# Kernel tuning notes

Measured on AMD Instinct MI355X. Metric: run time of the kernel, lower is better.

## Reference

```python
import jax, jax.numpy as jnp
import numpy as np

T_OUT = 12  # num_timesteps_output


def setup_inputs() -> dict:
    key = jax.random.key(0)
    ks = jax.random.split(key, 12)
    B, N, T, F = 32, 325, 12, 2
    C, H = 10, 64
    s = 0.08  # weight init scale (~1/sqrt(H)) to keep gates in sane range
    return {
        "A": jnp.zeros((N, N), jnp.float32),
        "X": jax.random.normal(ks[0], (B, N, T, F), jnp.float32),
        "enc_Wih": jax.random.normal(ks[1], (C, 3 * H, F), jnp.float32) * s,
        "enc_Whh": jax.random.normal(ks[2], (C, 3 * H, H), jnp.float32) * s,
        "enc_bih": jax.random.normal(ks[3], (C, 3 * H), jnp.float32) * s,
        "enc_bhh": jax.random.normal(ks[4], (C, 3 * H), jnp.float32) * s,
        "dec_Wih": jax.random.normal(ks[5], (C, 3 * H, 1), jnp.float32) * s,
        "dec_Whh": jax.random.normal(ks[6], (C, 3 * H, H), jnp.float32) * s,
        "dec_bih": jax.random.normal(ks[7], (C, 3 * H), jnp.float32) * s,
        "dec_bhh": jax.random.normal(ks[8], (C, 3 * H), jnp.float32) * s,
        "lin_W": jax.random.normal(ks[9], (C, 1, H), jnp.float32) * s,
        "lin_b": jax.random.normal(ks[10], (C, 1), jnp.float32) * s,
        "embed": jax.random.normal(ks[11], (N, C), jnp.float32),
    }


def _gru_update(gi, gh, h, H):
    # PyTorch GRU gate order: r, z, n
    r = jax.nn.sigmoid(gi[..., :H] + gh[..., :H])
    z = jax.nn.sigmoid(gi[..., H:2 * H] + gh[..., H:2 * H])
    n = jnp.tanh(gi[..., 2 * H:] + r * gh[..., 2 * H:])
    return (1.0 - z) * n + z * h


def reference(A, X, enc_Wih, enc_Whh, enc_bih, enc_bhh,
              dec_Wih, dec_Whh, dec_bih, dec_bhh, lin_W, lin_b, embed):
    B, N, T, F = X.shape
    C = enc_Wih.shape[0]
    H = enc_Whh.shape[-1]
    BN = B * N

    # (T, BN, F): time-major, batch*nodes flattened (matches X.view(-1,T,F).permute(1,0,2))
    Xs = jnp.transpose(X.reshape(BN, T, F), (1, 0, 2))

    def enc_step(h, x_t):  # h: (C, BN, H), x_t: (BN, F)
        gi = jnp.einsum('bf,cgf->cbg', x_t, enc_Wih) + enc_bih[:, None, :]
        gh = jnp.einsum('cbh,cgh->cbg', h, enc_Whh) + enc_bhh[:, None, :]
        return _gru_update(gi, gh, h, H), None

    h0 = jnp.zeros((C, BN, H), X.dtype)
    h_enc, _ = jax.lax.scan(enc_step, h0, Xs)  # (C, BN, H)

    # initial decoder input: last observed value of feature 0
    lv0 = jnp.broadcast_to(Xs[-1, :, 0][None, :, None], (C, BN, 1))

    def dec_step(carry, _):
        h, lv = carry
        gi = jnp.einsum('cbf,cgf->cbg', lv, dec_Wih) + dec_bih[:, None, :]
        gh = jnp.einsum('cbh,cgh->cbg', h, dec_Whh) + dec_bhh[:, None, :]
        h = _gru_update(gi, gh, h, H)
        value = jnp.einsum('cbh,coh->cbo', h, lin_W) + lin_b[:, None, :]  # (C, BN, 1)
        # original does last_value = value.detach()
        return (h, jax.lax.stop_gradient(value)), value

    (_, _), vals = jax.lax.scan(dec_step, (h_enc, lv0), None, length=T_OUT)
    # vals: (T_out, C, BN, 1) -> (B, N, T_out, C)
    out = jnp.transpose(vals[..., 0], (2, 0, 1)).reshape(B, N, T_OUT, C)

    weight = jax.nn.softmax(embed, axis=-1)  # (N, C)
    return jnp.einsum('bntc,nc->bnt', out, weight)
```

## Files before the change

kernel.cpp:

```cpp
#include <hip/hip_runtime.h>
#include <math.h>

#define N_     325
#define BN_    10400
#define OUTSZ_ (BN_*12)


typedef _Float16 h8v  __attribute__((ext_vector_type(8)));
typedef float    f4v  __attribute__((ext_vector_type(4)));
typedef unsigned int u32x4 __attribute__((ext_vector_type(4)));

#define L1C 1.4426950408889634f
#define L2C 2.8853900817779268f

__device__ __forceinline__ float rcp_f(float x){ return __builtin_amdgcn_rcpf(x); }
#if __has_builtin(__builtin_amdgcn_exp2f)
__device__ __forceinline__ float exp2_f(float x){ return __builtin_amdgcn_exp2f(x); }
#else
__device__ __forceinline__ float exp2_f(float x){ return __expf(x * 0.6931471805599453f); }
#endif

__device__ __forceinline__ unsigned short f16u(float x){
    union { _Float16 h; unsigned short u; } cv; cv.h = (_Float16)x; return cv.u;
}

#define BOFF   0
#define EOFF   24576
#define HOFF   27648
#define XOFF   36864
#define LWOFF  36864
#define WOFF   39936
#define LOFF   40192
#define SMEMSZ 40448

#define MFMA(A,B,C) __builtin_amdgcn_mfma_f32_16x16x32_f16((A),(B),(C),0,0,0)

__device__ __forceinline__ void stage_main(const float* __restrict__ W, char* smem, int tid)
{
    for (int it = 0; it < 24; ++it) {
        int q    = (it*256 + tid) * 2;
        int gc   = q >> 6;
        int k    = q & 63;
        int g    = gc >> 6;
        int colf = gc & 63;
        int f    = g*8 + (colf >> 4)*2 + (k >> 5);
        int lanew = ((k >> 3) & 3)*16 + (colf & 15);
        float sc = (g < 2) ? -L1C : -L2C;
        float2 wv = *(const float2*)(W + q);
        unsigned short* d = (unsigned short*)(smem + BOFF + f*1024 + lanew*16 + (k & 7)*2);
        d[0] = f16u(sc*wv.x);
        d[1] = f16u(sc*wv.y);
    }
}

__device__ __forceinline__ void rnn_step(h8v Aeh, h8v Ah0, h8v Ah1,
                                         const char* bb, const char* eb,
                                         const float cbh[4], float (&hreg)[4][4],
                                         char* wp)
{
    const f4v Z0 = {0.f,0.f,0.f,0.f};
#pragma unroll
    for (int ct = 0; ct < 4; ++ct) {
        f4v a0 = MFMA(Aeh, *(const h8v*)(eb + ct*256),       Z0);
        a0 = MFMA(Ah0, *(const h8v*)(bb + (ct*2   )*1024), a0);
        a0 = MFMA(Ah1, *(const h8v*)(bb + (ct*2+1 )*1024), a0);
        f4v a1 = MFMA(Aeh, *(const h8v*)(eb + (4+ct)*256),   Z0);
        a1 = MFMA(Ah0, *(const h8v*)(bb + (8+ct*2 )*1024), a1);
        a1 = MFMA(Ah1, *(const h8v*)(bb + (9+ct*2 )*1024), a1);
        f4v a3 = MFMA(Aeh, *(const h8v*)(eb + (8+ct)*256),   Z0);
        f4v a2 = MFMA(Ah0, *(const h8v*)(bb + (16+ct*2)*1024), Z0);
        a2 = MFMA(Ah1, *(const h8v*)(bb + (17+ct*2)*1024), a2);
#pragma unroll
        for (int i = 0; i < 4; ++i) {
            float er = exp2_f(a0[i]);
            float rr = rcp_f(1.0f + er);
            float ez = exp2_f(a1[i]);
            float en = exp2_f(fmaf(rr, a2[i] + cbh[ct], a3[i]));
            float h  = hreg[ct][i];
            float aa = 1.0f + ez;
            float den = fmaf(en, aa, aa);
            float t1  = fmaf(-en, ez, ez);
            float t2  = fmaf(en, h, h);
            float hnew = (t1 + t2) * rcp_f(den);
            hreg[ct][i] = hnew;
            *(_Float16*)(wp + i*144 + 32*ct) = (_Float16)hnew;
        }
    }
}

__global__ void __launch_bounds__(256, 4) krnn_kernel(
    const float* __restrict__ X,
    const float* __restrict__ eWih, const float* __restrict__ eWhh,
    const float* __restrict__ ebih, const float* __restrict__ ebhh,
    const float* __restrict__ dWih, const float* __restrict__ dWhh,
    const float* __restrict__ dbih, const float* __restrict__ dbhh,
    const float* __restrict__ linW, const float* __restrict__ linb,
    const float* __restrict__ embed, float* __restrict__ ws)
{
    __shared__ __align__(16) char smem[SMEMSZ];

    const int c    = blockIdx.y;
    const int row0 = blockIdx.x * 64;
    const int tid  = threadIdx.x;
    const int lane = tid & 63;
    const int w    = tid >> 6;
    const int l15  = lane & 15;
    const int kg   = lane >> 4;

    stage_main(eWhh + c*12288, smem, tid);

    if (tid < 192) {
        int e = tid >> 4, ln = tid & 15;
        int g = e >> 2, ct = e & 3;
        int gc = g*64 + ct*16 + ln;
        float sc = (g < 2) ? -L1C : -L2C;
        float w0 = eWih[c*384 + gc*2], w1 = eWih[c*384 + gc*2 + 1];
        float bb_ = (g < 2) ? (ebih[c*192+gc] + ebhh[c*192+gc]) : ebih[c*192+gc];
        unsigned short* d = (unsigned short*)(smem + EOFF + e*256 + ln*16);
        d[0] = f16u(sc*w0); d[1] = f16u(sc*w1); d[2] = f16u(sc*bb_);
        d[3]=0; d[4]=0; d[5]=0; d[6]=0; d[7]=0;
    }
    for (int i = tid; i < 768; i += 256) {
        int r = i / 12, t = i - r*12;
        int rg = row0 + r; if (rg >= BN_) rg = BN_-1;
        const float* p = X + (size_t)rg*24 + t*2;
        unsigned v = (unsigned)f16u(p[0]) | ((unsigned)f16u(p[1]) << 16);
        *(unsigned*)(smem + XOFF + r*48 + t*4) = v;
    }
    if (tid < 64) {
        int r = row0 + tid; if (r >= BN_) r = BN_-1;
        int n = r % N_;
        float e[10], mx = -1e30f;
#pragma unroll
        for (int cc=0; cc<10; ++cc){ e[cc]=embed[n*10+cc]; mx=fmaxf(mx,e[cc]); }
        float den = 0.0f;
#pragma unroll
        for (int cc=0; cc<10; ++cc) den += exp2_f((e[cc]-mx)*L1C);
        *(float*)(smem + WOFF + tid*4) = exp2_f((e[c]-mx)*L1C) * rcp_f(den);
    }
    for (int i = tid; i < 2304; i += 256)
        *(unsigned*)(smem + HOFF + i*4) = 0u;

    float cbh[4];
#pragma unroll
    for (int ct=0; ct<4; ++ct) cbh[ct] = -L2C * ebhh[c*192 + 128 + l15 + 16*ct];

    __syncthreads();

    float wreg[4];
#pragma unroll
    for (int i=0;i<4;++i) wreg[i] = *(const float*)(smem + WOFF + (w*16 + kg*4 + i)*4);

    char* hp = smem + HOFF + w*2304;
    const int rdo = l15*144 + kg*16;
    char* wp = hp + kg*576 + l15*2;
    const char* bb = smem + lane*16;
    const char* eb = smem + EOFF + l15*16;

    float hreg[4][4];
#pragma unroll
    for (int ct=0; ct<4; ++ct)
#pragma unroll
        for (int i=0;i<4;++i) hreg[ct][i] = 0.0f;

    for (int t = 0; t < 12; ++t) {
        unsigned xd = *(const unsigned*)(smem + XOFF + (w*16 + l15)*48 + t*4);
        union { u32x4 u; h8v h; } ae;
        ae.u.x = (lane < 16) ? xd : 0u;
        ae.u.y = (lane < 16) ? 0x00003C00u : 0u;
        ae.u.z = 0u; ae.u.w = 0u;
        h8v Ah0 = *(const h8v*)(hp + rdo);
        h8v Ah1 = *(const h8v*)(hp + rdo + 64);
        rnn_step(ae.h, Ah0, Ah1, bb, eb, cbh, hreg, wp);
    }

    unsigned aew = (*(const unsigned*)(smem + XOFF + (w*16 + l15)*48 + 44) & 0xFFFFu)
                   | 0x3C000000u;

    __syncthreads();

    stage_main(dWhh + c*12288, smem, tid);
    if (tid < 192) {
        int e = tid >> 4, ln = tid & 15;
        int g = e >> 2, ct = e & 3;
        int gc = g*64 + ct*16 + ln;
        float k0, k1;
        if (g < 2) { k0 = -L1C*dWih[c*192+gc]; k1 = -L1C*(dbih[c*192+gc]+dbhh[c*192+gc]); }
        else       { k0 = -L2C*dWih[c*192+gc]; k1 = -L2C*dbih[c*192+gc]; }
        unsigned short* d = (unsigned short*)(smem + EOFF + e*256 + ln*16);
        d[0] = f16u(k0); d[1] = f16u(k1);
        d[2]=0; d[3]=0; d[4]=0; d[5]=0; d[6]=0; d[7]=0;
    }
    if (tid < 128) {
        int ch = tid >> 6, ln = tid & 63;
        int kb = ch*32 + (ln >> 4)*8;
        unsigned short* d = (unsigned short*)(smem + LWOFF + ch*1024 + ln*16);
#pragma unroll
        for (int j=0;j<8;++j) d[j] = f16u(linW[c*64 + kb + j]);
    }
#pragma unroll
    for (int ct=0; ct<4; ++ct) cbh[ct] = -L2C * dbhh[c*192 + 128 + l15 + 16*ct];
    const float lb = linb[c];
    float* __restrict__ wsc = ws + (size_t)c * OUTSZ_;

    __syncthreads();

    for (int s = 0; s < 12; ++s) {
        h8v Ah0 = *(const h8v*)(hp + rdo);
        h8v Ah1 = *(const h8v*)(hp + rdo + 64);
        if (s > 0) {
            const f4v Zv = {0.f,0.f,0.f,0.f};
            f4v av = MFMA(Ah0, *(const h8v*)(smem + LWOFF + lane*16), Zv);
            av = MFMA(Ah1, *(const h8v*)(smem + LWOFF + 1024 + lane*16), av);
            if (l15 == 0) {
#pragma unroll
                for (int i=0;i<4;++i) {
                    float lv = av[i] + lb;
                    *(float*)(smem + LOFF + w*64 + (kg*4+i)*4) = lv;
                    int r = row0 + w*16 + kg*4 + i;
                    if (r < BN_) wsc[(size_t)r*12 + (s-1)] = wreg[i]*lv;
                }
            }
            float lvme = *(const float*)(smem + LOFF + w*64 + l15*4);
            aew = (unsigned)f16u(lvme) | 0x3C000000u;
        }
        union { u32x4 u; h8v h; } ae;
        ae.u.x = (lane < 16) ? aew : 0u;
        ae.u.y = 0u; ae.u.z = 0u; ae.u.w = 0u;
        rnn_step(ae.h, Ah0, Ah1, bb, eb, cbh, hreg, wp);
    }

    {
        h8v Ah0 = *(const h8v*)(hp + rdo);
        h8v Ah1 = *(const h8v*)(hp + rdo + 64);
        const f4v Zv = {0.f,0.f,0.f,0.f};
        f4v av = MFMA(Ah0, *(const h8v*)(smem + LWOFF + lane*16), Zv);
        av = MFMA(Ah1, *(const h8v*)(smem + LWOFF + 1024 + lane*16), av);
        if (l15 == 0) {
#pragma unroll
            for (int i=0;i<4;++i) {
                float lv = av[i] + lb;
                int r = row0 + w*16 + kg*4 + i;
                if (r < BN_) wsc[(size_t)r*12 + 11] = wreg[i]*lv;
            }
        }
    }
}

__global__ void __launch_bounds__(256) mix_kernel(const float* __restrict__ ws,
                                                  float* __restrict__ out)
{
    int i = blockIdx.x * 256 + threadIdx.x;
    if (i < OUTSZ_) {
        float s = 0.0f;
#pragma unroll
        for (int c = 0; c < 10; ++c) s += ws[(size_t)c * OUTSZ_ + i];
        out[i] = s;
    }
}

extern "C" void kernel_launch(void* const* d_in, const int* in_sizes, int n_in,
                              void* d_out, int out_size, void* d_ws, size_t ws_size,
                              hipStream_t stream) {
    const float* X    = (const float*)d_in[1];
    const float* eWih = (const float*)d_in[2];
    const float* eWhh = (const float*)d_in[3];
    const float* ebih = (const float*)d_in[4];
    const float* ebhh = (const float*)d_in[5];
    const float* dWih = (const float*)d_in[6];
    const float* dWhh = (const float*)d_in[7];
    const float* dbih = (const float*)d_in[8];
    const float* dbhh = (const float*)d_in[9];
    const float* linW = (const float*)d_in[10];
    const float* linb = (const float*)d_in[11];
    const float* emb  = (const float*)d_in[12];
    float* ws  = (float*)d_ws;
    float* out = (float*)d_out;

    dim3 grid((BN_ + 63) / 64, 10);
    krnn_kernel<<<grid, dim3(256), 0, stream>>>(
        X, eWih, eWhh, ebih, ebhh, dWih, dWhh, dbih, dbhh, linW, linb, emb, ws);
    mix_kernel<<<(OUTSZ_ + 255) / 256, dim3(256), 0, stream>>>(ws, out);
}
```

Measured before the change: 224.5 us.

## Keep recurrent GRU weight fragments in registers instead of shared memory

Each lane now loads its MFMA B-fragments of the hidden-to-hidden weights, and the output projection weights, straight from global memory into 24 h8v registers. Previously these were staged through LDS. Encoder and decoder input weights are staged up front in separate LDS regions, which removes the mid-kernel barrier and restaging, and shared memory shrinks to about 19 KB. The aim is to drop per-step LDS reads of the weight matrix from the recurrent loop. The cost is much higher VGPR pressure, so launch bounds fall from 4 to 2 blocks per CU, which lowers occupancy.

Measured after the change: 254.2 us. +13.2%, slower.

```diff
diff --git a/kernel.cpp b/kernel.cpp
--- a/kernel.cpp
+++ b/kernel.cpp
@@ -24,52 +24,56 @@
     union { _Float16 h; unsigned short u; } cv; cv.h = (_Float16)x; return cv.u;
 }
 
-#define BOFF   0
-#define EOFF   24576
-#define HOFF   27648
-#define XOFF   36864
-#define LWOFF  36864
-#define WOFF   39936
-#define LOFF   40192
-#define SMEMSZ 40448
+#define HOFF   0
+#define XOFF   9216
+#define EEOFF  12288
+#define EDOFF  15360
+#define WOFF   18432
+#define LOFF   18688
+#define SMEMSZ 18944
 
 #define MFMA(A,B,C) __builtin_amdgcn_mfma_f32_16x16x32_f16((A),(B),(C),0,0,0)
 
-__device__ __forceinline__ void stage_main(const float* __restrict__ W, char* smem, int tid)
-{
-    for (int it = 0; it < 24; ++it) {
-        int q    = (it*256 + tid) * 2;
-        int gc   = q >> 6;
-        int k    = q & 63;
-        int g    = gc >> 6;
-        int colf = gc & 63;
-        int f    = g*8 + (colf >> 4)*2 + (k >> 5);
-        int lanew = ((k >> 3) & 3)*16 + (colf & 15);
-        float sc = (g < 2) ? -L1C : -L2C;
-        float2 wv = *(const float2*)(W + q);
-        unsigned short* d = (unsigned short*)(smem + BOFF + f*1024 + lanew*16 + (k & 7)*2);
-        d[0] = f16u(sc*wv.x);
-        d[1] = f16u(sc*wv.y);
+__device__ __forceinline__ void load_frags(const float* __restrict__ W,
+                                           int l15, int kg, h8v (&F)[24])
+{
+#pragma unroll
+    for (int g=0; g<3; ++g) {
+        const float sc = (g<2) ? -L1C : -L2C;
+#pragma unroll
+        for (int ct=0; ct<4; ++ct)
+#pragma unroll
+            for (int ch=0; ch<2; ++ch) {
+                const float* p = W + (g*64 + ct*16 + l15)*64 + ch*32 + kg*8;
+                float4 a = *(const float4*)p;
+                float4 b = *(const float4*)(p+4);
+                h8v v;
+                v[0]=(_Float16)(sc*a.x); v[1]=(_Float16)(sc*a.y);
+                v[2]=(_Float16)(sc*a.z); v[3]=(_Float16)(sc*a.w);
+                v[4]=(_Float16)(sc*b.x); v[5]=(_Float16)(sc*b.y);
+                v[6]=(_Float16)(sc*b.z); v[7]=(_Float16)(sc*b.w);
+                F[g*8+ct*2+ch] = v;
+            }
     }
 }
 
 __device__ __forceinline__ void rnn_step(h8v Aeh, h8v Ah0, h8v Ah1,
-                                         const char* bb, const char* eb,
+                                         const h8v (&F)[24], const char* eb,
                                          const float cbh[4], float (&hreg)[4][4],
                                          char* wp)
 {
     const f4v Z0 = {0.f,0.f,0.f,0.f};
 #pragma unroll
     for (int ct = 0; ct < 4; ++ct) {
-        f4v a0 = MFMA(Aeh, *(const h8v*)(eb + ct*256),       Z0);
-        a0 = MFMA(Ah0, *(const h8v*)(bb + (ct*2   )*1024), a0);
-        a0 = MFMA(Ah1, *(const h8v*)(bb + (ct*2+1 )*1024), a0);
-        f4v a1 = MFMA(Aeh, *(const h8v*)(eb + (4+ct)*256),   Z0);
-        a1 = MFMA(Ah0, *(const h8v*)(bb + (8+ct*2 )*1024), a1);
-        a1 = MFMA(Ah1, *(const h8v*)(bb + (9+ct*2 )*1024), a1);
-        f4v a3 = MFMA(Aeh, *(const h8v*)(eb + (8+ct)*256),   Z0);
-        f4v a2 = MFMA(Ah0, *(const h8v*)(bb + (16+ct*2)*1024), Z0);
-        a2 = MFMA(Ah1, *(const h8v*)(bb + (17+ct*2)*1024), a2);
+        f4v a0 = MFMA(Aeh, *(const h8v*)(eb + ct*256), Z0);
+        a0 = MFMA(Ah0, F[ct*2  ], a0);
+        a0 = MFMA(Ah1, F[ct*2+1], a0);
+        f4v a1 = MFMA(Aeh, *(const h8v*)(eb + (4+ct)*256), Z0);
+        a1 = MFMA(Ah0, F[8+ct*2], a1);
+        a1 = MFMA(Ah1, F[9+ct*2], a1);
+        f4v a3 = MFMA(Aeh, *(const h8v*)(eb + (8+ct)*256), Z0);
+        f4v a2 = MFMA(Ah0, F[16+ct*2], Z0);
+        a2 = MFMA(Ah1, F[17+ct*2], a2);
 #pragma unroll
         for (int i = 0; i < 4; ++i) {
             float er = exp2_f(a0[i]);
@@ -88,7 +92,7 @@
     }
 }
 
-__global__ void __launch_bounds__(256, 4) krnn_kernel(
+__global__ void __launch_bounds__(256, 2) krnn_kernel(
     const float* __restrict__ X,
     const float* __restrict__ eWih, const float* __restrict__ eWhh,
     const float* __restrict__ ebih, const float* __restrict__ ebhh,
@@ -107,25 +111,34 @@
     const int l15  = lane & 15;
     const int kg   = lane >> 4;
 
-    stage_main(eWhh + c*12288, smem, tid);
-
+    for (int i = tid; i < 768; i += 256) {
+        int r = i / 12, t = i - r*12;
+        int rg = row0 + r; if (rg >= BN_) rg = BN_-1;
+        const float* p = X + (size_t)rg*24 + t*2;
+        unsigned v = (unsigned)f16u(p[0]) | ((unsigned)f16u(p[1]) << 16);
+        *(unsigned*)(smem + XOFF + r*48 + t*4) = v;
+    }
     if (tid < 192) {
         int e = tid >> 4, ln = tid & 15;
         int g = e >> 2, ct = e & 3;
         int gc = g*64 + ct*16 + ln;
         float sc = (g < 2) ? -L1C : -L2C;
         float w0 = eWih[c*384 + gc*2], w1 = eWih[c*384 + gc*2 + 1];
-        float bb_ = (g < 2) ? (ebih[c*192+gc] + ebhh[c*192+gc]) : ebih[c*192+gc];
-        unsigned short* d = (unsigned short*)(smem + EOFF + e*256 + ln*16);
-        d[0] = f16u(sc*w0); d[1] = f16u(sc*w1); d[2] = f16u(sc*bb_);
+        float bb = (g < 2) ? (ebih[c*192+gc] + ebhh[c*192+gc]) : ebih[c*192+gc];
+        unsigned short* d = (unsigned short*)(smem + EEOFF + e*256 + ln*16);
+        d[0] = f16u(sc*w0); d[1] = f16u(sc*w1); d[2] = f16u(sc*bb);
         d[3]=0; d[4]=0; d[5]=0; d[6]=0; d[7]=0;
     }
-    for (int i = tid; i < 768; i += 256) {
-        int r = i / 12, t = i - r*12;
-        int rg = row0 + r; if (rg >= BN_) rg = BN_-1;
-        const float* p = X + (size_t)rg*24 + t*2;
-        unsigned v = (unsigned)f16u(p[0]) | ((unsigned)f16u(p[1]) << 16);
-        *(unsigned*)(smem + XOFF + r*48 + t*4) = v;
+    if (tid < 192) {
+        int e = tid >> 4, ln = tid & 15;
+        int g = e >> 2, ct = e & 3;
+        int gc = g*64 + ct*16 + ln;
+        float k0, k1;
+        if (g < 2) { k0 = -L1C*dWih[c*192+gc]; k1 = -L1C*(dbih[c*192+gc]+dbhh[c*192+gc]); }
+        else       { k0 = -L2C*dWih[c*192+gc]; k1 = -L2C*dbih[c*192+gc]; }
+        unsigned short* d = (unsigned short*)(smem + EDOFF + e*256 + ln*16);
+        d[0] = f16u(k0); d[1] = f16u(k1);
+        d[2]=0; d[3]=0; d[4]=0; d[5]=0; d[6]=0; d[7]=0;
     }
     if (tid < 64) {
         int r = row0 + tid; if (r >= BN_) r = BN_-1;
@@ -141,10 +154,6 @@
     for (int i = tid; i < 2304; i += 256)
         *(unsigned*)(smem + HOFF + i*4) = 0u;
 
-    float cbh[4];
-#pragma unroll
-    for (int ct=0; ct<4; ++ct) cbh[ct] = -L2C * ebhh[c*192 + 128 + l15 + 16*ct];
-
     __syncthreads();
 
     float wreg[4];
@@ -154,8 +163,15 @@
     char* hp = smem + HOFF + w*2304;
     const int rdo = l15*144 + kg*16;
     char* wp = hp + kg*576 + l15*2;
-    const char* bb = smem + lane*16;
-    const char* eb = smem + EOFF + l15*16;
+    const char* ebE = smem + EEOFF + l15*16;
+    const char* ebD = smem + EDOFF + l15*16;
+
+    h8v F[24];
+    load_frags(eWhh + c*12288, l15, kg, F);
+
+    float cbh[4];
+#pragma unroll
+    for (int ct=0; ct<4; ++ct) cbh[ct] = -L2C * ebhh[c*192 + 128 + l15 + 16*ct];
 
     float hreg[4][4];
 #pragma unroll
@@ -171,47 +187,36 @@
         ae.u.z = 0u; ae.u.w = 0u;
         h8v Ah0 = *(const h8v*)(hp + rdo);
         h8v Ah1 = *(const h8v*)(hp + rdo + 64);
-        rnn_step(ae.h, Ah0, Ah1, bb, eb, cbh, hreg, wp);
+        rnn_step(ae.h, Ah0, Ah1, F, ebE, cbh, hreg, wp);
     }
 
     unsigned aew = (*(const unsigned*)(smem + XOFF + (w*16 + l15)*48 + 44) & 0xFFFFu)
                    | 0x3C000000u;
 
-    __syncthreads();
-
-    stage_main(dWhh + c*12288, smem, tid);
-    if (tid < 192) {
-        int e = tid >> 4, ln = tid & 15;
-        int g = e >> 2, ct = e & 3;
-        int gc = g*64 + ct*16 + ln;
-        float k0, k1;
-        if (g < 2) { k0 = -L1C*dWih[c*192+gc]; k1 = -L1C*(dbih[c*192+gc]+dbhh[c*192+gc]); }
-        else       { k0 = -L2C*dWih[c*192+gc]; k1 = -L2C*dbih[c*192+gc]; }
-        unsigned short* d = (unsigned short*)(smem + EOFF + e*256 + ln*16);
-        d[0] = f16u(k0); d[1] = f16u(k1);
-        d[2]=0; d[3]=0; d[4]=0; d[5]=0; d[6]=0; d[7]=0;
-    }
-    if (tid < 128) {
-        int ch = tid >> 6, ln = tid & 63;
-        int kb = ch*32 + (ln >> 4)*8;
-        unsigned short* d = (unsigned short*)(smem + LWOFF + ch*1024 + ln*16);
-#pragma unroll
-        for (int j=0;j<8;++j) d[j] = f16u(linW[c*64 + kb + j]);
+    load_frags(dWhh + c*12288, l15, kg, F);
+    h8v Blw[2];
+#pragma unroll
+    for (int ch=0; ch<2; ++ch) {
+        const float* p = linW + c*64 + ch*32 + kg*8;
+        float4 a = *(const float4*)p;
+        float4 b = *(const float4*)(p+4);
+        h8v v;
+        v[0]=(_Float16)a.x; v[1]=(_Float16)a.y; v[2]=(_Float16)a.z; v[3]=(_Float16)a.w;
+        v[4]=(_Float16)b.x; v[5]=(_Float16)b.y; v[6]=(_Float16)b.z; v[7]=(_Float16)b.w;
+        Blw[ch] = v;
     }
 #pragma unroll
     for (int ct=0; ct<4; ++ct) cbh[ct] = -L2C * dbhh[c*192 + 128 + l15 + 16*ct];
     const float lb = linb[c];
     float* __restrict__ wsc = ws + (size_t)c * OUTSZ_;
-
-    __syncthreads();
 
     for (int s = 0; s < 12; ++s) {
         h8v Ah0 = *(const h8v*)(hp + rdo);
         h8v Ah1 = *(const h8v*)(hp + rdo + 64);
         if (s > 0) {
             const f4v Zv = {0.f,0.f,0.f,0.f};
-            f4v av = MFMA(Ah0, *(const h8v*)(smem + LWOFF + lane*16), Zv);
-            av = MFMA(Ah1, *(const h8v*)(smem + LWOFF + 1024 + lane*16), av);
+            f4v av = MFMA(Ah0, Blw[0], Zv);
+            av = MFMA(Ah1, Blw[1], av);
             if (l15 == 0) {
 #pragma unroll
                 for (int i=0;i<4;++i) {
@@ -227,15 +232,15 @@
         union { u32x4 u; h8v h; } ae;
         ae.u.x = (lane < 16) ? aew : 0u;
         ae.u.y = 0u; ae.u.z = 0u; ae.u.w = 0u;
-        rnn_step(ae.h, Ah0, Ah1, bb, eb, cbh, hreg, wp);
+        rnn_step(ae.h, Ah0, Ah1, F, ebD, cbh, hreg, wp);
     }
 
     {
         h8v Ah0 = *(const h8v*)(hp + rdo);
         h8v Ah1 = *(const h8v*)(hp + rdo + 64);
         const f4v Zv = {0.f,0.f,0.f,0.f};
-        f4v av = MFMA(Ah0, *(const h8v*)(smem + LWOFF + lane*16), Zv);
-        av = MFMA(Ah1, *(const h8v*)(smem + LWOFF + 1024 + lane*16), av);
+        f4v av = MFMA(Ah0, Blw[0], Zv);
+        av = MFMA(Ah1, Blw[1], av);
         if (l15 == 0) {
 #pragma unroll
             for (int i=0;i<4;++i) {
```

## Double rows per block to 128 with 512 threads and vectorize weight staging

Applied to the files above, without the earlier changes.

Each block now handles 128 rows with 8 waves instead of 64 rows with 4 waves, so the per-cluster weight staging into LDS is shared by twice as many rows. The staging loop is rewritten to do vectorized float4 loads and 16-byte LDS stores. The linear-layer weights are kept in registers instead of LDS. The trade-off is more LDS per block, fewer blocks (820 vs 1630), and more register pressure under the new 512-thread launch bounds, which could lower occupancy or cause spills.

Result: slower. 232.5 us (+3.6%).

```diff
diff --git a/kernel.cpp b/kernel.cpp
--- a/kernel.cpp
+++ b/kernel.cpp
@@ -4,6 +4,7 @@
 #define N_     325
 #define BN_    10400
 #define OUTSZ_ (BN_*12)
+#define RB_    128
 
 
 typedef _Float16 h8v  __attribute__((ext_vector_type(8)));
@@ -27,29 +28,37 @@
 #define BOFF   0
 #define EOFF   24576
 #define HOFF   27648
-#define XOFF   36864
-#define LWOFF  36864
-#define WOFF   39936
-#define LOFF   40192
-#define SMEMSZ 40448
+#define XOFF   46080
+#define WOFF   52224
+#define LOFF   52736
+#define SMEMSZ 53248
 
 #define MFMA(A,B,C) __builtin_amdgcn_mfma_f32_16x16x32_f16((A),(B),(C),0,0,0)
 
 __device__ __forceinline__ void stage_main(const float* __restrict__ W, char* smem, int tid)
 {
-    for (int it = 0; it < 24; ++it) {
-        int q    = (it*256 + tid) * 2;
-        int gc   = q >> 6;
-        int k    = q & 63;
-        int g    = gc >> 6;
-        int colf = gc & 63;
-        int f    = g*8 + (colf >> 4)*2 + (k >> 5);
-        int lanew = ((k >> 3) & 3)*16 + (colf & 15);
-        float sc = (g < 2) ? -L1C : -L2C;
-        float2 wv = *(const float2*)(W + q);
-        unsigned short* d = (unsigned short*)(smem + BOFF + f*1024 + lanew*16 + (k & 7)*2);
-        d[0] = f16u(sc*wv.x);
-        d[1] = f16u(sc*wv.y);
+#pragma unroll
+    for (int it = 0; it < 3; ++it) {
+        int a16   = it*512 + tid;
+        int f     = a16 >> 6;
+        int lanew = a16 & 63;
+        int colf  = lanew & 15;
+        int kb4   = lanew >> 4;
+        int ch    = f & 1;
+        int ct    = (f >> 1) & 3;
+        int g     = f >> 3;
+        int gc    = g*64 + ct*16 + colf;
+        int k0    = ch*32 + kb4*8;
+        float sc  = (g < 2) ? -L1C : -L2C;
+        const float* p = W + gc*64 + k0;
+        float4 a = *(const float4*)p;
+        float4 b = *(const float4*)(p+4);
+        h8v v;
+        v[0]=(_Float16)(sc*a.x); v[1]=(_Float16)(sc*a.y);
+        v[2]=(_Float16)(sc*a.z); v[3]=(_Float16)(sc*a.w);
+        v[4]=(_Float16)(sc*b.x); v[5]=(_Float16)(sc*b.y);
+        v[6]=(_Float16)(sc*b.z); v[7]=(_Float16)(sc*b.w);
+        *(h8v*)(smem + BOFF + a16*16) = v;
     }
 }
 
@@ -88,7 +97,7 @@
     }
 }
 
-__global__ void __launch_bounds__(256, 4) krnn_kernel(
+__global__ void __launch_bounds__(512, 6) krnn_kernel(
     const float* __restrict__ X,
     const float* __restrict__ eWih, const float* __restrict__ eWhh,
     const float* __restrict__ ebih, const float* __restrict__ ebhh,
@@ -100,7 +109,7 @@
     __shared__ __align__(16) char smem[SMEMSZ];
 
     const int c    = blockIdx.y;
-    const int row0 = blockIdx.x * 64;
+    const int row0 = blockIdx.x * RB_;
     const int tid  = threadIdx.x;
     const int lane = tid & 63;
     const int w    = tid >> 6;
@@ -120,14 +129,14 @@
         d[0] = f16u(sc*w0); d[1] = f16u(sc*w1); d[2] = f16u(sc*bb_);
         d[3]=0; d[4]=0; d[5]=0; d[6]=0; d[7]=0;
     }
-    for (int i = tid; i < 768; i += 256) {
+    for (int i = tid; i < RB_*12; i += 512) {
         int r = i / 12, t = i - r*12;
         int rg = row0 + r; if (rg >= BN_) rg = BN_-1;
         const float* p = X + (size_t)rg*24 + t*2;
         unsigned v = (unsigned)f16u(p[0]) | ((unsigned)f16u(p[1]) << 16);
         *(unsigned*)(smem + XOFF + r*48 + t*4) = v;
     }
-    if (tid < 64) {
+    if (tid < RB_) {
         int r = row0 + tid; if (r >= BN_) r = BN_-1;
         int n = r % N_;
         float e[10], mx = -1e30f;
@@ -138,7 +147,7 @@
         for (int cc=0; cc<10; ++cc) den += exp2_f((e[cc]-mx)*L1C);
         *(float*)(smem + WOFF + tid*4) = exp2_f((e[c]-mx)*L1C) * rcp_f(den);
     }
-    for (int i = tid; i < 2304; i += 256)
+    for (int i = tid; i < 4608; i += 512)
         *(unsigned*)(smem + HOFF + i*4) = 0u;
 
     float cbh[4];
@@ -191,12 +200,16 @@
         d[0] = f16u(k0); d[1] = f16u(k1);
         d[2]=0; d[3]=0; d[4]=0; d[5]=0; d[6]=0; d[7]=0;
     }
-    if (tid < 128) {
-        int ch = tid >> 6, ln = tid & 63;
-        int kb = ch*32 + (ln >> 4)*8;
-        unsigned short* d = (unsigned short*)(smem + LWOFF + ch*1024 + ln*16);
-#pragma unroll
-        for (int j=0;j<8;++j) d[j] = f16u(linW[c*64 + kb + j]);
+    h8v Blw[2];
+#pragma unroll
+    for (int ch=0; ch<2; ++ch) {
+        const float* p = linW + c*64 + ch*32 + kg*8;
+        float4 a = *(const float4*)p;
+        float4 b = *(const float4*)(p+4);
+        h8v v;
+        v[0]=(_Float16)a.x; v[1]=(_Float16)a.y; v[2]=(_Float16)a.z; v[3]=(_Float16)a.w;
+        v[4]=(_Float16)b.x; v[5]=(_Float16)b.y; v[6]=(_Float16)b.z; v[7]=(_Float16)b.w;
+        Blw[ch] = v;
     }
 #pragma unroll
     for (int ct=0; ct<4; ++ct) cbh[ct] = -L2C * dbhh[c*192 + 128 + l15 + 16*ct];
@@ -210,8 +223,8 @@
         h8v Ah1 = *(const h8v*)(hp + rdo + 64);
         if (s > 0) {
             const f4v Zv = {0.f,0.f,0.f,0.f};
-            f4v av = MFMA(Ah0, *(const h8v*)(smem + LWOFF + lane*16), Zv);
-            av = MFMA(Ah1, *(const h8v*)(smem + LWOFF + 1024 + lane*16), av);
+            f4v av = MFMA(Ah0, Blw[0], Zv);
+            av = MFMA(Ah1, Blw[1], av);
             if (l15 == 0) {
 #pragma unroll
                 for (int i=0;i<4;++i) {
@@ -234,8 +247,8 @@
         h8v Ah0 = *(const h8v*)(hp + rdo);
         h8v Ah1 = *(const h8v*)(hp + rdo + 64);
         const f4v Zv = {0.f,0.f,0.f,0.f};
-        f4v av = MFMA(Ah0, *(const h8v*)(smem + LWOFF + lane*16), Zv);
-        av = MFMA(Ah1, *(const h8v*)(smem + LWOFF + 1024 + lane*16), av);
+        f4v av = MFMA(Ah0, Blw[0], Zv);
+        av = MFMA(Ah1, Blw[1], av);
         if (l15 == 0) {
 #pragma unroll
             for (int i=0;i<4;++i) {
@@ -277,8 +290,8 @@
     float* ws  = (float*)d_ws;
     float* out = (float*)d_out;
 
-    dim3 grid((BN_ + 63) / 64, 10);
-    krnn_kernel<<<grid, dim3(256), 0, stream>>>(
+    dim3 grid((BN_ + RB_ - 1) / RB_, 10);
+    krnn_kernel<<<grid, dim3(512), 0, stream>>>(
         X, eWih, eWhh, ebih, ebhh, dWih, dWhh, dbih, dbhh, linW, linb, emb, ws);
     mix_kernel<<<(OUTSZ_ + 255) / 256, dim3(256), 0, stream>>>(ws, out);
 }
```
